# Kernel optimization log

Measured on AMD Instinct MI355X. Metric: run time of the kernel, lower is better.

Reference implementation:

```python
import jax, jax.numpy as jnp
import numpy as np
from jax import lax

BATCH = 8192
HID = 10
IN = 64
STEPS = 512
REVERSE = True


def setup_inputs() -> dict:
    key = jax.random.key(0)
    ks = jax.random.split(key, 9)
    s_in = 1.0 / np.sqrt(HID)
    return {
        "hidden": jax.random.normal(ks[0], (1, BATCH, HID), dtype=jnp.float32),
        "w_ih": jax.random.uniform(ks[1], (3 * HID, IN), jnp.float32, -s_in, s_in),
        "w_hh": jax.random.uniform(ks[2], (3 * HID, HID), jnp.float32, -s_in, s_in),
        "b_ih": jax.random.uniform(ks[3], (3 * HID,), jnp.float32, -s_in, s_in),
        "b_hh": jax.random.uniform(ks[4], (3 * HID,), jnp.float32, -s_in, s_in),
        "l1_w": jax.random.uniform(ks[5], (10, HID), jnp.float32, -s_in, s_in),
        "l1_b": jax.random.uniform(ks[6], (10,), jnp.float32, -s_in, s_in),
        "l2_w": jax.random.uniform(ks[7], (IN, 10), jnp.float32, -s_in, s_in),
        "l2_b": jax.random.uniform(ks[8], (IN,), jnp.float32, -s_in, s_in),
        "step": STEPS,
    }


def _gru_cell(h, x, w_ih, w_hh, b_ih, b_hh):
    # PyTorch GRU gate order: reset, update, new
    gi = x @ w_ih.T + b_ih  # [B, 3H]
    gh = h @ w_hh.T + b_hh  # [B, 3H]
    i_r, i_z, i_n = jnp.split(gi, 3, axis=-1)
    h_r, h_z, h_n = jnp.split(gh, 3, axis=-1)
    r = jax.nn.sigmoid(i_r + h_r)
    z = jax.nn.sigmoid(i_z + h_z)
    n = jnp.tanh(i_n + r * h_n)
    return (1.0 - z) * n + z * h


def reference(hidden, w_ih, w_hh, b_ih, b_hh, l1_w, l1_b, l2_w, l2_b, step):
    h0 = hidden[0]  # [B, H]
    B = h0.shape[0]
    x0 = jnp.zeros((B, IN), dtype=h0.dtype)  # first GRU input is zeros

    def body(carry, _):
        h, x = carry
        h_new = _gru_cell(h, x, w_ih, w_hh, b_ih, b_hh)
        o = h_new @ l1_w.T + l1_b          # l1 on GRU output
        x_next = o @ l2_w.T + l2_b         # l2 feeds next GRU step
        return (h_new, x_next), o

    _, outs = lax.scan(body, (h0, x0), None, length=step)  # [T, B, 10]
    outs = jnp.transpose(outs, (1, 0, 2))  # [B, T, 10]
    if REVERSE:
        outs = outs[:, ::-1, :]
    return outs
```

## Files before the change

### kernel.cpp

```cpp
#include <hip/hip_runtime.h>

#define HID 10
#define STEPS 512

typedef __attribute__((ext_vector_type(2))) float v2f;

template<int F>
static __device__ __forceinline__ float swz(float v) {
    return __int_as_float(__builtin_amdgcn_ds_swizzle(__float_as_int(v), (F << 5) | 0x10));
}

__global__ __launch_bounds__(64, 2) void gru_decoder_kernel(
    const float* __restrict__ hidden, const float* __restrict__ w_ih,
    const float* __restrict__ w_hh, const float* __restrict__ b_ih,
    const float* __restrict__ b_hh, const float* __restrict__ l1_w,
    const float* __restrict__ l1_b, const float* __restrict__ l2_w,
    const float* __restrict__ l2_b, float* __restrict__ out)
{
    __shared__ float sWx[640];
    __shared__ float sbx[64];
    __shared__ float sWgi[300];
    __shared__ float sbgi[30];
    __shared__ float sWhh[300];

    const int lane = threadIdx.x;
    const int f    = lane & 15;
    const int b    = blockIdx.x * 4 + (lane >> 4);
    const bool ok  = (f < HID);
    const int fi   = ok ? f : 0;

    for (int e = lane; e < 640; e += 64) {
        int i = e / 10, j = e - i * 10;
        float acc = 0.f;
        #pragma unroll
        for (int k = 0; k < 10; ++k) acc += l2_w[i * 10 + k] * l1_w[k * 10 + j];
        sWx[e] = acc;
    }
    {
        float acc = l2_b[lane];
        #pragma unroll
        for (int k = 0; k < 10; ++k) acc += l2_w[lane * 10 + k] * l1_b[k];
        sbx[lane] = acc;
    }
    for (int e = lane; e < 300; e += 64) sWhh[e] = w_hh[e];
    __syncthreads();
    for (int e = lane; e < 300; e += 64) {
        int m = e / 10, j = e - m * 10;
        float acc = 0.f;
        for (int k = 0; k < 64; ++k) acc += w_ih[m * 64 + k] * sWx[k * 10 + j];
        sWgi[e] = acc;
    }
    if (lane < 30) {
        float acc = b_ih[lane];
        for (int k = 0; k < 64; ++k) acc += w_ih[lane * 64 + k] * sbx[k];
        sbgi[lane] = acc;
    }
    __syncthreads();

    const float LOG2E = 1.4426950408889634f;
    const float S2    = 2.f * LOG2E;

    v2f wrz[10], wnn[10];
    float wo[10];
    #pragma unroll
    for (int k = 0; k < 10; ++k) {
        float grz_r = -(sWgi[fi * 10 + k] + sWhh[fi * 10 + k]) * LOG2E;
        float grz_z = -(sWgi[(10 + fi) * 10 + k] + sWhh[(10 + fi) * 10 + k]) * LOG2E;
        float gni   = sWgi[(20 + fi) * 10 + k] * S2;
        float gnh   = sWhh[(20 + fi) * 10 + k] * S2;
        wrz[k] = ok ? v2f{grz_r, grz_z} : v2f{0.f, 0.f};
        wnn[k] = ok ? v2f{gni, gnh} : v2f{0.f, 0.f};
        wo[k]  = ok ? l1_w[fi * 10 + k] : 0.f;
    }
    const v2f brz = ok ? v2f{-(sbgi[fi] + b_hh[fi]) * LOG2E,
                             -(sbgi[10 + fi] + b_hh[10 + fi]) * LOG2E}
                       : v2f{0.f, 0.f};
    const v2f bnn = ok ? v2f{sbgi[20 + fi] * S2, b_hh[20 + fi] * S2} : v2f{0.f, 0.f};
    const float bo = ok ? l1_b[fi] : 0.f;
    const v2f brz0 = ok ? v2f{-(b_ih[fi] + b_hh[fi]) * LOG2E,
                              -(b_ih[10 + fi] + b_hh[10 + fi]) * LOG2E}
                        : v2f{0.f, 0.f};
    const float bni0 = ok ? b_ih[20 + fi] * S2 : 0.f;

    float h = ok ? hidden[(size_t)b * HID + f] : 0.f;

    float ha[10];
    #define GATHER()                                                       \
        ha[0] = swz<0>(h); ha[1] = swz<1>(h); ha[2] = swz<2>(h);           \
        ha[3] = swz<3>(h); ha[4] = swz<4>(h); ha[5] = swz<5>(h);           \
        ha[6] = swz<6>(h); ha[7] = swz<7>(h); ha[8] = swz<8>(h);           \
        ha[9] = swz<9>(h);

    GATHER();

    float* pb = out + (size_t)b * (STEPS * HID) + (size_t)(STEPS - 1) * HID + f;

    #define O_AND_STORE()                                                  \
        {                                                                  \
            float o = bo;                                                  \
            _Pragma("unroll")                                              \
            for (int k = 0; k < 10; ++k) o += wo[k] * ha[k];               \
            if (ok) pb[0] = o;                                             \
            pb -= HID;                                                     \
        }

    {
        float pr = 0.f, pz = 0.f, ph = 0.f;
        #pragma unroll
        for (int k = 0; k < 10; ++k) {
            pr += sWhh[fi * 10 + k] * ha[k];
            pz += sWhh[(10 + fi) * 10 + k] * ha[k];
            ph += sWhh[(20 + fi) * 10 + k] * ha[k];
        }
        float vr = brz0.x - pr * LOG2E;
        float vz = brz0.y - pz * LOG2E;
        float r = __builtin_amdgcn_rcpf(1.f + __builtin_amdgcn_exp2f(vr));
        float z = __builtin_amdgcn_rcpf(1.f + __builtin_amdgcn_exp2f(vz));
        float y = bni0 + r * (ph * S2 + bnn.y);
        float n = 1.f - 2.f * __builtin_amdgcn_rcpf(1.f + __builtin_amdgcn_exp2f(y));
        h = ok ? (n + z * (h - n)) : 0.f;
        GATHER();
        O_AND_STORE();
    }

    #pragma unroll 1
    for (int t = 1; t < STEPS; ++t) {
        v2f arz = brz, ann = bnn;
        #pragma unroll
        for (int k = 0; k < 10; ++k) {
            v2f hh = {ha[k], ha[k]};
            arz += wrz[k] * hh;
            ann += wnn[k] * hh;
        }
        float r = __builtin_amdgcn_rcpf(1.f + __builtin_amdgcn_exp2f(arz.x));
        float z = __builtin_amdgcn_rcpf(1.f + __builtin_amdgcn_exp2f(arz.y));
        float y = ann.x + r * ann.y;
        float n = 1.f - 2.f * __builtin_amdgcn_rcpf(1.f + __builtin_amdgcn_exp2f(y));
        h = n + z * (h - n);
        GATHER();
        O_AND_STORE();
    }
}

extern "C" void kernel_launch(void* const* d_in, const int* in_sizes, int n_in,
                              void* d_out, int out_size, void* d_ws, size_t ws_size,
                              hipStream_t stream) {
    (void)in_sizes; (void)n_in; (void)d_ws; (void)ws_size; (void)out_size;
    dim3 grid(2048), block(64);
    gru_decoder_kernel<<<grid, block, 0, stream>>>(
        (const float*)d_in[0], (const float*)d_in[1], (const float*)d_in[2],
        (const float*)d_in[3], (const float*)d_in[4], (const float*)d_in[5],
        (const float*)d_in[6], (const float*)d_in[7], (const float*)d_in[8],
        (float*)d_out);
}
```

Baseline: 315.3 us.

## Stage outputs in LDS for coalesced 8-byte stores and use packed FMA

Outputs are buffered in shared memory for 16 timesteps per batch row, then written out as contiguous 8-byte non-temporal stores. This replaces one scattered 4-byte store per step. Gate and output dot products are restructured into explicit v_pk_fma_f32 pairs over the hidden dimension, followed by a horizontal add. This adds LDS traffic and relies on a single wavefront for ordering between the LDS writes and reads, with no barrier.

Result: slower. 330.4 us (+4.8%).

```diff
diff --git a/kernel.cpp b/kernel.cpp
--- a/kernel.cpp
+++ b/kernel.cpp
@@ -8,6 +8,15 @@
 template<int F>
 static __device__ __forceinline__ float swz(float v) {
     return __int_as_float(__builtin_amdgcn_ds_swizzle(__float_as_int(v), (F << 5) | 0x10));
+}
+
+static __device__ __forceinline__ v2f pk_mul(v2f a, v2f b) {
+    v2f d;
+    asm("v_pk_mul_f32 %0, %1, %2" : "=v"(d) : "v"(a), "v"(b));
+    return d;
+}
+static __device__ __forceinline__ void pk_fma(v2f& acc, v2f a, v2f b) {
+    asm("v_pk_fma_f32 %0, %1, %2, %0" : "+v"(acc) : "v"(a), "v"(b));
 }
 
 __global__ __launch_bounds__(64, 2) void gru_decoder_kernel(
@@ -22,10 +31,12 @@
     __shared__ float sWgi[300];
     __shared__ float sbgi[30];
     __shared__ float sWhh[300];
+    __shared__ alignas(16) float sstage[4 * 168];
 
     const int lane = threadIdx.x;
     const int f    = lane & 15;
-    const int b    = blockIdx.x * 4 + (lane >> 4);
+    const int grp  = lane >> 4;
+    const int b    = blockIdx.x * 4 + grp;
     const bool ok  = (f < HID);
     const int fi   = ok ? f : 0;
 
@@ -60,51 +71,65 @@
     const float LOG2E = 1.4426950408889634f;
     const float S2    = 2.f * LOG2E;
 
-    v2f wrz[10], wnn[10];
-    float wo[10];
+    v2f wr2[5], wz2[5], wni2[5], wnh2[5], wo2[5];
     #pragma unroll
-    for (int k = 0; k < 10; ++k) {
-        float grz_r = -(sWgi[fi * 10 + k] + sWhh[fi * 10 + k]) * LOG2E;
-        float grz_z = -(sWgi[(10 + fi) * 10 + k] + sWhh[(10 + fi) * 10 + k]) * LOG2E;
-        float gni   = sWgi[(20 + fi) * 10 + k] * S2;
-        float gnh   = sWhh[(20 + fi) * 10 + k] * S2;
-        wrz[k] = ok ? v2f{grz_r, grz_z} : v2f{0.f, 0.f};
-        wnn[k] = ok ? v2f{gni, gnh} : v2f{0.f, 0.f};
-        wo[k]  = ok ? l1_w[fi * 10 + k] : 0.f;
+    for (int i = 0; i < 5; ++i) {
+        int k0 = 2 * i, k1 = 2 * i + 1;
+        if (ok) {
+            wr2[i]  = (v2f){-(sWgi[fi * 10 + k0] + sWhh[fi * 10 + k0]) * LOG2E,
+                            -(sWgi[fi * 10 + k1] + sWhh[fi * 10 + k1]) * LOG2E};
+            wz2[i]  = (v2f){-(sWgi[(10 + fi) * 10 + k0] + sWhh[(10 + fi) * 10 + k0]) * LOG2E,
+                            -(sWgi[(10 + fi) * 10 + k1] + sWhh[(10 + fi) * 10 + k1]) * LOG2E};
+            wni2[i] = (v2f){sWgi[(20 + fi) * 10 + k0] * S2, sWgi[(20 + fi) * 10 + k1] * S2};
+            wnh2[i] = (v2f){sWhh[(20 + fi) * 10 + k0] * S2, sWhh[(20 + fi) * 10 + k1] * S2};
+            wo2[i]  = (v2f){l1_w[fi * 10 + k0], l1_w[fi * 10 + k1]};
+        } else {
+            v2f zz = {0.f, 0.f};
+            wr2[i] = zz; wz2[i] = zz; wni2[i] = zz; wnh2[i] = zz; wo2[i] = zz;
+        }
     }
-    const v2f brz = ok ? v2f{-(sbgi[fi] + b_hh[fi]) * LOG2E,
-                             -(sbgi[10 + fi] + b_hh[10 + fi]) * LOG2E}
-                       : v2f{0.f, 0.f};
-    const v2f bnn = ok ? v2f{sbgi[20 + fi] * S2, b_hh[20 + fi] * S2} : v2f{0.f, 0.f};
-    const float bo = ok ? l1_b[fi] : 0.f;
-    const v2f brz0 = ok ? v2f{-(b_ih[fi] + b_hh[fi]) * LOG2E,
-                              -(b_ih[10 + fi] + b_hh[10 + fi]) * LOG2E}
-                        : v2f{0.f, 0.f};
+    const float br  = ok ? -(sbgi[fi] + b_hh[fi]) * LOG2E : 0.f;
+    const float bz  = ok ? -(sbgi[10 + fi] + b_hh[10 + fi]) * LOG2E : 0.f;
+    const float bni = ok ? sbgi[20 + fi] * S2 : 0.f;
+    const float bnh = ok ? b_hh[20 + fi] * S2 : 0.f;
+    const float bo  = ok ? l1_b[fi] : 0.f;
+    const float br0  = ok ? -(b_ih[fi] + b_hh[fi]) * LOG2E : 0.f;
+    const float bz0  = ok ? -(b_ih[10 + fi] + b_hh[10 + fi]) * LOG2E : 0.f;
     const float bni0 = ok ? b_ih[20 + fi] * S2 : 0.f;
 
     float h = ok ? hidden[(size_t)b * HID + f] : 0.f;
 
-    float ha[10];
-    #define GATHER()                                                       \
-        ha[0] = swz<0>(h); ha[1] = swz<1>(h); ha[2] = swz<2>(h);           \
-        ha[3] = swz<3>(h); ha[4] = swz<4>(h); ha[5] = swz<5>(h);           \
-        ha[6] = swz<6>(h); ha[7] = swz<7>(h); ha[8] = swz<8>(h);           \
-        ha[9] = swz<9>(h);
+    v2f h2[5];
+    #define GATHER()                                             \
+        h2[0] = (v2f){swz<0>(h), swz<1>(h)};                     \
+        h2[1] = (v2f){swz<2>(h), swz<3>(h)};                     \
+        h2[2] = (v2f){swz<4>(h), swz<5>(h)};                     \
+        h2[3] = (v2f){swz<6>(h), swz<7>(h)};                     \
+        h2[4] = (v2f){swz<8>(h), swz<9>(h)};
 
     GATHER();
 
-    float* pb = out + (size_t)b * (STEPS * HID) + (size_t)(STEPS - 1) * HID + f;
+    float* wp = ok ? &sstage[grp * 168 + 150 + f] : &sstage[grp * 168 + 166];
+    const int vdec = ok ? 10 : 0;
+    const int vinc = vdec * 16;
+    float* pf = out + (size_t)b * (STEPS * HID) + (size_t)(STEPS - 16) * HID + 2 * f;
+    const int rb = grp * 168 + 2 * f;
 
-    #define O_AND_STORE()                                                  \
-        {                                                                  \
-            float o = bo;                                                  \
-            _Pragma("unroll")                                              \
-            for (int k = 0; k < 10; ++k) o += wo[k] * ha[k];               \
-            if (ok) pb[0] = o;                                             \
-            pb -= HID;                                                     \
+    #define O_WRITE()                                            \
+        {                                                        \
+            v2f ao = pk_mul(wo2[0], h2[0]);                      \
+            pk_fma(ao, wo2[1], h2[1]);                           \
+            pk_fma(ao, wo2[2], h2[2]);                           \
+            pk_fma(ao, wo2[3], h2[3]);                           \
+            pk_fma(ao, wo2[4], h2[4]);                           \
+            *wp = ao.x + ao.y + bo;                              \
+            wp -= vdec;                                          \
         }
 
     {
+        float ha[10];
+        #pragma unroll
+        for (int i = 0; i < 5; ++i) { ha[2 * i] = h2[i].x; ha[2 * i + 1] = h2[i].y; }
         float pr = 0.f, pz = 0.f, ph = 0.f;
         #pragma unroll
         for (int k = 0; k < 10; ++k) {
@@ -112,33 +137,49 @@
             pz += sWhh[(10 + fi) * 10 + k] * ha[k];
             ph += sWhh[(20 + fi) * 10 + k] * ha[k];
         }
-        float vr = brz0.x - pr * LOG2E;
-        float vz = brz0.y - pz * LOG2E;
+        float vr = br0 - pr * LOG2E;
+        float vz = bz0 - pz * LOG2E;
         float r = __builtin_amdgcn_rcpf(1.f + __builtin_amdgcn_exp2f(vr));
         float z = __builtin_amdgcn_rcpf(1.f + __builtin_amdgcn_exp2f(vz));
-        float y = bni0 + r * (ph * S2 + bnn.y);
+        float y = bni0 + r * (ph * S2 + bnh);
         float n = 1.f - 2.f * __builtin_amdgcn_rcpf(1.f + __builtin_amdgcn_exp2f(y));
         h = ok ? (n + z * (h - n)) : 0.f;
         GATHER();
-        O_AND_STORE();
+        O_WRITE();
     }
 
     #pragma unroll 1
     for (int t = 1; t < STEPS; ++t) {
-        v2f arz = brz, ann = bnn;
+        v2f ar = pk_mul(wr2[0], h2[0]);
+        v2f az = pk_mul(wz2[0], h2[0]);
+        v2f ai = pk_mul(wni2[0], h2[0]);
+        v2f ah = pk_mul(wnh2[0], h2[0]);
         #pragma unroll
-        for (int k = 0; k < 10; ++k) {
-            v2f hh = {ha[k], ha[k]};
-            arz += wrz[k] * hh;
-            ann += wnn[k] * hh;
+        for (int i = 1; i < 5; ++i) {
+            pk_fma(ar, wr2[i], h2[i]);
+            pk_fma(az, wz2[i], h2[i]);
+            pk_fma(ai, wni2[i], h2[i]);
+            pk_fma(ah, wnh2[i], h2[i]);
         }
-        float r = __builtin_amdgcn_rcpf(1.f + __builtin_amdgcn_exp2f(arz.x));
-        float z = __builtin_amdgcn_rcpf(1.f + __builtin_amdgcn_exp2f(arz.y));
-        float y = ann.x + r * ann.y;
+        float vr = (ar.x + ar.y) + br;
+        float vz = (az.x + az.y) + bz;
+        float r = __builtin_amdgcn_rcpf(1.f + __builtin_amdgcn_exp2f(vr));
+        float z = __builtin_amdgcn_rcpf(1.f + __builtin_amdgcn_exp2f(vz));
+        float y = ((ai.x + ai.y) + bni) + r * ((ah.x + ah.y) + bnh);
         float n = 1.f - 2.f * __builtin_amdgcn_rcpf(1.f + __builtin_amdgcn_exp2f(y));
         h = n + z * (h - n);
         GATHER();
-        O_AND_STORE();
+        O_WRITE();
+
+        if ((t & 15) == 15) {
+            #pragma unroll
+            for (int c = 0; c < 5; ++c) {
+                v2f v = *reinterpret_cast<const v2f*>(&sstage[rb + 32 * c]);
+                __builtin_nontemporal_store(v, reinterpret_cast<v2f*>(pf + 32 * c));
+            }
+            pf -= 16 * HID;
+            wp += vinc;
+        }
     }
 }
 
```
